# Kernel tuning notes

Hardware: AMD Instinct MI355X
Metric: run time of the kernel (lower is better)

The kernel has to match this reference:

```python
import jax, jax.numpy as jnp
import numpy as np

N = 100000      # nodes
E = 1600000     # edges (avg degree 16)
IN_DIM = 128
OUT_DIM = 64


def setup_inputs() -> dict:
    key = jax.random.key(0)
    k1, k2, k3, k4, k5 = jax.random.split(key, 5)
    h = jax.random.normal(k1, (N, IN_DIM), dtype=jnp.float32)
    W = jax.random.normal(k2, (IN_DIM, OUT_DIM), dtype=jnp.float32) * 0.05
    a = jax.random.normal(k3, (2 * OUT_DIM,), dtype=jnp.float32) * 0.05
    src = jax.random.randint(k4, (E,), 0, N, dtype=jnp.int32)
    dst = jax.random.randint(k5, (E,), 0, N, dtype=jnp.int32)
    return {"h": h, "W": W, "a": a, "src": src, "dst": dst}


def reference(h, W, a, src, dst):
    # z = W h  (node projection)
    z = h @ W                                   # [N, D]
    # Edge attention: e_ij = leaky_relu(a^T [z_i || z_j])
    # decomposed: a = [a_src; a_dst] -> e = leaky_relu(<z_src,a_src>+<z_dst,a_dst>)
    a_src, a_dst = a[:OUT_DIM], a[OUT_DIM:]
    s_src = z @ a_src                           # [N]
    s_dst = z @ a_dst                           # [N]
    e = jax.nn.leaky_relu(s_src[src] + s_dst[dst])  # [E], slope 0.01 (torch default)
    # Segmented softmax over incoming edges of each dst node
    m = jax.ops.segment_max(e, dst, num_segments=N)       # [N]
    m = jnp.where(jnp.isneginf(m), 0.0, m)                # empty mailboxes
    ex = jnp.exp(e - m[dst])                              # [E]
    denom = jax.ops.segment_sum(ex, dst, num_segments=N)  # [N]
    alpha = ex / jnp.where(denom == 0.0, 1.0, denom)[dst] # [E]
    # Weighted sum of source messages per dst node
    out = jax.ops.segment_sum(alpha[:, None] * z[src], dst, num_segments=N)  # [N, D]
    return out
```

## Files before the change

### kernel.cpp

```cpp
#include <hip/hip_runtime.h>
#include <math.h>

#define NN   100000
#define NE   1600000
#define IND  128
#define OUTD 64

#define BK_NODES 64
#define NBUCK    1563
#define CAPB     1280
#define CAPN     64

#define OFF_Z      0
#define OFF_SSRC   (OFF_Z + NN * OUTD / 2)
#define OFF_SDST   (OFF_SSRC + NN)
#define OFF_BCNT   (OFF_SDST + NN)
#define OFF_COARSE (OFF_BCNT + NBUCK)

typedef __bf16 bf16x8 __attribute__((ext_vector_type(8)));
typedef unsigned short u16x8 __attribute__((ext_vector_type(8)));
typedef float f32x4 __attribute__((ext_vector_type(4)));

union FragU { u16x8 u; bf16x8 b; };

__device__ __forceinline__ unsigned short f32_to_bf16_rne(float x)
{
    unsigned int b = __float_as_uint(x);
    b += 0x7FFFu + ((b >> 16) & 1u);
    return (unsigned short)(b >> 16);
}

#define WLPAD 136

__global__ void __launch_bounds__(256) k_zs(
    const float* __restrict__ h, const float* __restrict__ W,
    const float* __restrict__ a, unsigned short* __restrict__ z16,
    float* __restrict__ s_src, float* __restrict__ s_dst)
{
    __shared__ __attribute__((aligned(16))) unsigned short WL[OUTD * WLPAD];
    int t = threadIdx.x;

    for (int idx = t; idx < IND * OUTD; idx += 256) {
        int k = idx >> 6;
        int c = idx & 63;
        WL[c * WLPAD + k] = f32_to_bf16_rne(W[idx]);
    }
    __syncthreads();

    int lane = t & 63;
    int wave = t >> 6;
    int c = lane & 15;
    int g = lane >> 4;

    FragU bf[4][4];
#pragma unroll
    for (int ks = 0; ks < 4; ++ks)
#pragma unroll
        for (int nt = 0; nt < 4; ++nt)
            bf[ks][nt].u = *reinterpret_cast<const u16x8*>(
                &WL[(nt * 16 + c) * WLPAD + ks * 32 + g * 8]);

    int rbase = blockIdx.x * 64 + wave * 16;
    int rowA = rbase + c;
    int rowAc = rowA < NN ? rowA : NN - 1;
    const float* hrow = h + rowAc * IND;

    FragU af[4];
#pragma unroll
    for (int ks = 0; ks < 4; ++ks) {
        float4 p = *reinterpret_cast<const float4*>(hrow + ks * 32 + g * 8);
        float4 q = *reinterpret_cast<const float4*>(hrow + ks * 32 + g * 8 + 4);
        u16x8 u;
        u[0] = f32_to_bf16_rne(p.x); u[1] = f32_to_bf16_rne(p.y);
        u[2] = f32_to_bf16_rne(p.z); u[3] = f32_to_bf16_rne(p.w);
        u[4] = f32_to_bf16_rne(q.x); u[5] = f32_to_bf16_rne(q.y);
        u[6] = f32_to_bf16_rne(q.z); u[7] = f32_to_bf16_rne(q.w);
        af[ks].u = u;
    }

    f32x4 acc[4];
#pragma unroll
    for (int nt = 0; nt < 4; ++nt) acc[nt] = (f32x4){0.f, 0.f, 0.f, 0.f};

#pragma unroll
    for (int nt = 0; nt < 4; ++nt)
#pragma unroll
        for (int ks = 0; ks < 4; ++ks)
            acc[nt] = __builtin_amdgcn_mfma_f32_16x16x32_bf16(
                af[ks].b, bf[ks][nt].b, acc[nt], 0, 0, 0);

    float as[4], ad[4];
#pragma unroll
    for (int nt = 0; nt < 4; ++nt) {
        as[nt] = a[nt * 16 + c];
        ad[nt] = a[OUTD + nt * 16 + c];
    }

#pragma unroll
    for (int reg = 0; reg < 4; ++reg) {
        int row = rbase + g * 4 + reg;
        float p1 = 0.f, p2 = 0.f;
#pragma unroll
        for (int nt = 0; nt < 4; ++nt) {
            float v = acc[nt][reg];
            p1 = fmaf(v, as[nt], p1);
            p2 = fmaf(v, ad[nt], p2);
            if (row < NN)
                z16[row * OUTD + nt * 16 + c] = f32_to_bf16_rne(v);
        }
#pragma unroll
        for (int mm = 1; mm < 16; mm <<= 1) {
            p1 += __shfl_xor(p1, mm, 64);
            p2 += __shfl_xor(p2, mm, 64);
        }
        if (c == 0 && row < NN) {
            s_src[row] = p1;
            s_dst[row] = p2;
        }
    }
}

#define BIN_THREADS 1024
#define BIN_EPT     4
#define BIN_BLOCKS  391

__global__ void __launch_bounds__(BIN_THREADS) k_bin(
    const int* __restrict__ src, const int* __restrict__ dst,
    int* __restrict__ bcnt, unsigned int* __restrict__ coarse)
{
    __shared__ int lhist[NBUCK];
    __shared__ int lbase[NBUCK];
    int t = threadIdx.x;

    for (int i = t; i < NBUCK; i += BIN_THREADS) lhist[i] = 0;
    __syncthreads();

    int sv[BIN_EPT], dv[BIN_EPT];
    bool val[BIN_EPT];
#pragma unroll
    for (int i = 0; i < BIN_EPT; ++i) {
        int e = blockIdx.x * (BIN_THREADS * BIN_EPT) + i * BIN_THREADS + t;
        val[i] = e < NE;
        sv[i] = 0; dv[i] = 0;
        if (val[i]) { sv[i] = src[e]; dv[i] = dst[e]; }
    }
#pragma unroll
    for (int i = 0; i < BIN_EPT; ++i)
        if (val[i]) atomicAdd(&lhist[dv[i] >> 6], 1);
    __syncthreads();

    for (int i = t; i < NBUCK; i += BIN_THREADS) {
        int c = lhist[i];
        lbase[i] = c ? atomicAdd(&bcnt[i], c) : 0;
        lhist[i] = 0;
    }
    __syncthreads();

#pragma unroll
    for (int i = 0; i < BIN_EPT; ++i) {
        if (val[i]) {
            int b = dv[i] >> 6;
            int r = atomicAdd(&lhist[b], 1);
            coarse[b * CAPB + lbase[b] + r] =
                ((unsigned int)sv[i] << 6) | (unsigned int)(dv[i] & 63);
        }
    }
}

__global__ void __launch_bounds__(512) k_node(
    const unsigned short* __restrict__ z16, const unsigned int* __restrict__ coarse,
    const int* __restrict__ bcnt, const float* __restrict__ s_src,
    const float* __restrict__ s_dst, float* __restrict__ out)
{
    __shared__ unsigned int seg[BK_NODES * CAPN];
    __shared__ int cnt[BK_NODES];
    int b = blockIdx.x;
    int t = threadIdx.x;

    if (t < BK_NODES) cnt[t] = 0;
    __syncthreads();

    int nb = bcnt[b];
    if (nb > CAPB) nb = CAPB;
    const unsigned int* cb = coarse + b * CAPB;
    for (int i = t; i < nb; i += 512) {
        unsigned int v = cb[i];
        int dl = (int)(v & 63u);
        int s  = (int)(v >> 6);
        int r = atomicAdd(&cnt[dl], 1);
        if (r < CAPN) seg[dl * CAPN + r] = s;
    }
    __syncthreads();

    int wave = t >> 6;
    int lane = t & 63;
    int eslot = lane >> 4;
    int cbase = (lane & 15) * 4;

    for (int ni = wave; ni < BK_NODES; ni += 8) {
        int node = b * BK_NODES + ni;
        if (node >= NN) continue;
        int d = cnt[ni];
        if (d > CAPN) d = CAPN;
        if (d == 0) {
            if (eslot == 0)
                *reinterpret_cast<float4*>(out + node * OUTD + cbase) =
                    make_float4(0.f, 0.f, 0.f, 0.f);
            continue;
        }
        float sdst = s_dst[node];

        int sid = 0;
        float ev = -INFINITY;
        if (lane < d) {
            sid = (int)seg[ni * CAPN + lane];
            float e0 = s_src[sid] + sdst;
            ev = e0 > 0.f ? e0 : 0.01f * e0;
        }
        int rowoff = sid * OUTD;

        float m = ev;
#pragma unroll
        for (int mm = 32; mm; mm >>= 1) m = fmaxf(m, __shfl_xor(m, mm, 64));
        float ex = (lane < d) ? __expf(ev - m) : 0.f;
        float l = ex;
#pragma unroll
        for (int mm = 32; mm; mm >>= 1) l += __shfl_xor(l, mm, 64);

        float a0 = 0.f, a1 = 0.f, a2 = 0.f, a3 = 0.f;
#pragma unroll 4
        for (int tt = 0; tt < d; tt += 4) {
            int e = tt + eslot;
            int ro = __shfl(rowoff, e, 64);
            float exv = __shfl(ex, e, 64);
            uint2 v = *reinterpret_cast<const uint2*>(z16 + ro + cbase);
            float f0 = __uint_as_float(v.x << 16);
            float f1 = __uint_as_float(v.x & 0xFFFF0000u);
            float f2 = __uint_as_float(v.y << 16);
            float f3 = __uint_as_float(v.y & 0xFFFF0000u);
            a0 = fmaf(exv, f0, a0);
            a1 = fmaf(exv, f1, a1);
            a2 = fmaf(exv, f2, a2);
            a3 = fmaf(exv, f3, a3);
        }

        a0 += __shfl_xor(a0, 16, 64); a0 += __shfl_xor(a0, 32, 64);
        a1 += __shfl_xor(a1, 16, 64); a1 += __shfl_xor(a1, 32, 64);
        a2 += __shfl_xor(a2, 16, 64); a2 += __shfl_xor(a2, 32, 64);
        a3 += __shfl_xor(a3, 16, 64); a3 += __shfl_xor(a3, 32, 64);

        if (eslot == 0) {
            float inv = 1.f / l;
            *reinterpret_cast<float4*>(out + node * OUTD + cbase) =
                make_float4(a0 * inv, a1 * inv, a2 * inv, a3 * inv);
        }
    }
}

extern "C" void kernel_launch(void* const* d_in, const int* in_sizes, int n_in,
                              void* d_out, int out_size, void* d_ws, size_t ws_size,
                              hipStream_t stream)
{
    const float* h   = (const float*)d_in[0];
    const float* W   = (const float*)d_in[1];
    const float* a   = (const float*)d_in[2];
    const int*   src = (const int*)d_in[3];
    const int*   dst = (const int*)d_in[4];
    float* out = (float*)d_out;

    int* ws_i = (int*)d_ws;

    unsigned short* z16 = (unsigned short*)(ws_i + OFF_Z);
    float* s_src  = (float*)(ws_i + OFF_SSRC);
    float* s_dst  = (float*)(ws_i + OFF_SDST);
    int*   bcnt   = ws_i + OFF_BCNT;
    unsigned int* coarse = (unsigned int*)(ws_i + OFF_COARSE);

    hipMemsetAsync(bcnt, 0, NBUCK * sizeof(int), stream);

    k_bin<<<BIN_BLOCKS, BIN_THREADS, 0, stream>>>(src, dst, bcnt, coarse);

    k_zs<<<(NN + 63) / 64, 256, 0, stream>>>(h, W, a, z16, s_src, s_dst);

    k_node<<<NBUCK, 512, 0, stream>>>(z16, coarse, bcnt, s_src, s_dst, out);
}
```

Measured before the change: 106.1 us.

## Pre-swizzle W into MFMA fragment layout once and stage h tile coalesced via LDS

The bf16 conversion and fragment swizzle of W now happen once, in block 0 of the binning kernel, and are written to a workspace buffer. Each k_zs block then loads its B fragments directly from that buffer instead of rebuilding W in LDS in every block. The h tile is now read with fully coalesced float4 loads, converted to bf16 and staged in LDS, and A fragments are read from there. This removes 1563 redundant W conversions and the strided per-lane h loads, at the cost of an extra sync, LDS traffic, and a dependency on k_bin running first.

```diff
diff --git a/kernel.cpp b/kernel.cpp
--- a/kernel.cpp
+++ b/kernel.cpp
@@ -15,7 +15,8 @@
 #define OFF_SSRC   (OFF_Z + NN * OUTD / 2)
 #define OFF_SDST   (OFF_SSRC + NN)
 #define OFF_BCNT   (OFF_SDST + NN)
-#define OFF_COARSE (OFF_BCNT + NBUCK)
+#define OFF_WSW    (OFF_BCNT + NBUCK)
+#define OFF_COARSE (OFF_WSW + 4096)
 
 typedef __bf16 bf16x8 __attribute__((ext_vector_type(8)));
 typedef unsigned short u16x8 __attribute__((ext_vector_type(8)));
@@ -33,19 +34,28 @@
 #define WLPAD 136
 
 __global__ void __launch_bounds__(256) k_zs(
-    const float* __restrict__ h, const float* __restrict__ W,
+    const float* __restrict__ h, const unsigned short* __restrict__ wsw,
     const float* __restrict__ a, unsigned short* __restrict__ z16,
     float* __restrict__ s_src, float* __restrict__ s_dst)
 {
-    __shared__ __attribute__((aligned(16))) unsigned short WL[OUTD * WLPAD];
+    __shared__ __attribute__((aligned(16))) unsigned short HL[64 * WLPAD];
     int t = threadIdx.x;
-
-    for (int idx = t; idx < IND * OUTD; idx += 256) {
-        int k = idx >> 6;
-        int c = idx & 63;
-        WL[c * WLPAD + k] = f32_to_bf16_rne(W[idx]);
-    }
-    __syncthreads();
+    int base = blockIdx.x * 64;
+
+    const float4* hg = reinterpret_cast<const float4*>(h);
+#pragma unroll
+    for (int i = 0; i < 8; ++i) {
+        int idx = i * 256 + t;
+        int r = idx >> 5;
+        int c4 = idx & 31;
+        float4 v = make_float4(0.f, 0.f, 0.f, 0.f);
+        if (base + r < NN) v = hg[(base + r) * 32 + c4];
+        unsigned int lo = (unsigned int)f32_to_bf16_rne(v.x) |
+                          ((unsigned int)f32_to_bf16_rne(v.y) << 16);
+        unsigned int hi = (unsigned int)f32_to_bf16_rne(v.z) |
+                          ((unsigned int)f32_to_bf16_rne(v.w) << 16);
+        *reinterpret_cast<uint2*>(&HL[r * WLPAD + c4 * 4]) = make_uint2(lo, hi);
+    }
 
     int lane = t & 63;
     int wave = t >> 6;
@@ -58,25 +68,15 @@
 #pragma unroll
         for (int nt = 0; nt < 4; ++nt)
             bf[ks][nt].u = *reinterpret_cast<const u16x8*>(
-                &WL[(nt * 16 + c) * WLPAD + ks * 32 + g * 8]);
-
-    int rbase = blockIdx.x * 64 + wave * 16;
-    int rowA = rbase + c;
-    int rowAc = rowA < NN ? rowA : NN - 1;
-    const float* hrow = h + rowAc * IND;
+                &wsw[((ks * 4 + nt) * 64 + lane) * 8]);
+
+    __syncthreads();
 
     FragU af[4];
 #pragma unroll
-    for (int ks = 0; ks < 4; ++ks) {
-        float4 p = *reinterpret_cast<const float4*>(hrow + ks * 32 + g * 8);
-        float4 q = *reinterpret_cast<const float4*>(hrow + ks * 32 + g * 8 + 4);
-        u16x8 u;
-        u[0] = f32_to_bf16_rne(p.x); u[1] = f32_to_bf16_rne(p.y);
-        u[2] = f32_to_bf16_rne(p.z); u[3] = f32_to_bf16_rne(p.w);
-        u[4] = f32_to_bf16_rne(q.x); u[5] = f32_to_bf16_rne(q.y);
-        u[6] = f32_to_bf16_rne(q.z); u[7] = f32_to_bf16_rne(q.w);
-        af[ks].u = u;
-    }
+    for (int ks = 0; ks < 4; ++ks)
+        af[ks].u = *reinterpret_cast<const u16x8*>(
+            &HL[(wave * 16 + c) * WLPAD + ks * 32 + g * 8]);
 
     f32x4 acc[4];
 #pragma unroll
@@ -89,6 +89,7 @@
             acc[nt] = __builtin_amdgcn_mfma_f32_16x16x32_bf16(
                 af[ks].b, bf[ks][nt].b, acc[nt], 0, 0, 0);
 
+    int rbase = base + wave * 16;
     float as[4], ad[4];
 #pragma unroll
     for (int nt = 0; nt < 4; ++nt) {
@@ -126,11 +127,24 @@
 
 __global__ void __launch_bounds__(BIN_THREADS) k_bin(
     const int* __restrict__ src, const int* __restrict__ dst,
+    const float* __restrict__ W, unsigned short* __restrict__ wsw,
     int* __restrict__ bcnt, unsigned int* __restrict__ coarse)
 {
     __shared__ int lhist[NBUCK];
     __shared__ int lbase[NBUCK];
     int t = threadIdx.x;
+
+    if (blockIdx.x == 0) {
+        int ks = t >> 8;
+        int nt = (t >> 6) & 3;
+        int lane = t & 63;
+        int g = lane >> 4, c = lane & 15;
+        u16x8 u;
+#pragma unroll
+        for (int j = 0; j < 8; ++j)
+            u[j] = f32_to_bf16_rne(W[(ks * 32 + g * 8 + j) * OUTD + nt * 16 + c]);
+        *reinterpret_cast<u16x8*>(&wsw[((ks * 4 + nt) * 64 + lane) * 8]) = u;
+    }
 
     for (int i = t; i < NBUCK; i += BIN_THREADS) lhist[i] = 0;
     __syncthreads();
@@ -274,13 +288,14 @@
     float* s_src  = (float*)(ws_i + OFF_SSRC);
     float* s_dst  = (float*)(ws_i + OFF_SDST);
     int*   bcnt   = ws_i + OFF_BCNT;
+    unsigned short* wsw = (unsigned short*)(ws_i + OFF_WSW);
     unsigned int* coarse = (unsigned int*)(ws_i + OFF_COARSE);
 
     hipMemsetAsync(bcnt, 0, NBUCK * sizeof(int), stream);
 
-    k_bin<<<BIN_BLOCKS, BIN_THREADS, 0, stream>>>(src, dst, bcnt, coarse);
-
-    k_zs<<<(NN + 63) / 64, 256, 0, stream>>>(h, W, a, z16, s_src, s_dst);
+    k_bin<<<BIN_BLOCKS, BIN_THREADS, 0, stream>>>(src, dst, W, wsw, bcnt, coarse);
+
+    k_zs<<<(NN + 63) / 64, 256, 0, stream>>>(h, wsw, a, z16, s_src, s_dst);
 
     k_node<<<NBUCK, 512, 0, stream>>>(z16, coarse, bcnt, s_src, s_dst, out);
 }
```

Result: faster. 103.2 us (-2.7%).
